# Performance work log

Hardware: AMD Instinct MI355X
Metric: run time of the kernel (lower is better)

Reference implementation:

```python
import jax, jax.numpy as jnp
import numpy as np

ALPHA = 1.0
BETA = 6.0
GAMMA = 1.0
N_DATA = 50000
IS_MSS = True
LOG2PI = float(np.log(2.0 * np.pi))


def _log_density_gaussian(x, mu, logvar):
    # elementwise Gaussian log-density
    return -0.5 * (LOG2PI + logvar) - 0.5 * (x - mu) ** 2 * jnp.exp(-logvar)


def _log_importance_weight_matrix(batch_size, n_data):
    # Faithful to the reference torch implementation (incl. the column-1 and
    # [M-1,0] stratified-weight overwrites done via flat strided assignment).
    N = float(n_data)
    M = float(batch_size - 1)
    strat = (N - M) / (N * M)
    W = jnp.full((batch_size, batch_size), 1.0 / M, dtype=jnp.float32)
    idx = jnp.arange(batch_size)
    W = W.at[idx, idx].set(1.0 / N)
    W = W.at[:, 1].set(strat)
    W = W.at[batch_size - 2, 0].set(strat)
    return jnp.log(W)


def setup_inputs() -> dict:
    key = jax.random.key(0)
    k1, k2, k3, k4, k5 = jax.random.split(key, 5)
    B, D = 1024, 64
    return {
        "recon_x": jax.random.normal(k1, (B, 3, 64, 64), dtype=jnp.float32),
        "x": jax.random.normal(k2, (B, 3, 64, 64), dtype=jnp.float32),
        "mu": jax.random.normal(k3, (B, D), dtype=jnp.float32),
        "logvar": jax.random.normal(k4, (B, D), dtype=jnp.float32),
        "noise": jax.random.normal(k5, (B, D), dtype=jnp.float32),
    }


def reference(recon_x, x, mu, logvar, noise):
    B, D = mu.shape
    # reconstruction: MSE with sum reduction
    reconstruction_loss = jnp.sum((recon_x - x) ** 2)

    # reparameterized latent sample (noise supplied deterministically)
    z = mu + noise * jnp.exp(0.5 * logvar)

    # log q(z|x) and log p(z), each summed over latent dims -> [B]
    log_q_zCx = _log_density_gaussian(z, mu, logvar).sum(axis=1)
    log_pz = _log_density_gaussian(z, jnp.zeros_like(z), jnp.zeros_like(z)).sum(axis=1)

    # pairwise matrix log q(z_i | x_j): [B, B, D]
    mat_log_qz = _log_density_gaussian(z[:, None, :], mu[None, :, :], logvar[None, :, :])
    if IS_MSS:
        log_iw = _log_importance_weight_matrix(B, N_DATA)
        mat_log_qz = mat_log_qz + log_iw[:, :, None]

    log_qz = jax.scipy.special.logsumexp(mat_log_qz.sum(axis=2), axis=1)  # [B]
    log_prod_qzi = jax.scipy.special.logsumexp(mat_log_qz, axis=1).sum(axis=1)  # [B]

    mi_loss = jnp.mean(log_q_zCx - log_qz)
    tc_loss = jnp.mean(log_qz - log_prod_qzi)
    dw_kl_loss = jnp.mean(log_prod_qzi - log_pz)

    return reconstruction_loss + (ALPHA * mi_loss + BETA * tc_loss + GAMMA * dw_kl_loss)
```

## Files before the change

kernel.cpp:

```cpp
#include <hip/hip_runtime.h>
#include <math.h>

typedef __attribute__((ext_vector_type(8))) short short8;
typedef __attribute__((ext_vector_type(4))) float f32x4;

#define BB 1024
#define DD 64
#define NPIX (1024*3*64*64)

#define LN2PI_F  1.8378770664093453f
#define LOG2E_F  1.4426950408889634f

#define INV_M  (1.0f/1023.0f)
#define INV_N  (1.0f/50000.0f)
#define STRATF ((float)((50000.0-1023.0)/(50000.0*1023.0)))
#define NEGBIG (-3.0e38f)

#define L2_INVM  (-9.9985904f)
#define L2_INVN  (-15.6096405f)
#define L2_STRAT (-10.0284195f)

#define WS_RP    0
#define WS_LQC   2048
#define WS_LPZ   3072
#define WS_LQZ   4096
#define WS_LPR   5120
#define WS_Z     6144
#define WS_Z2    71680
#define WS_A     137216
#define WS_B     202752
#define WS_C     268288
#define WS_KC    333824
#define WS_QZP   334848
#define WS_SEDP  400384
#define WS_ABF   924672
#define WS_BBF   990208

#define NB_RECON 1536
#define NB_PREP  256
#define RECON_REPS 8

#define NB_MM    256
#define NB_SED   1024

__device__ __forceinline__ float fexp2(float x){ return __builtin_amdgcn_exp2f(x); }
__device__ __forceinline__ float flog2(float x){ return __builtin_amdgcn_logf(x); }
__device__ __forceinline__ unsigned short tobf(float f){
    unsigned int u = __float_as_uint(f);
    u = (u + 0x7FFFu + ((u >> 16) & 1u)) >> 16;
    return (unsigned short)u;
}
__device__ __forceinline__ unsigned long long ld_agent(const unsigned long long* p) {
    return __hip_atomic_load(p, __ATOMIC_RELAXED, __HIP_MEMORY_SCOPE_AGENT);
}

__global__ __launch_bounds__(256) void k_reconprep(const float* __restrict__ rx,
                                                   const float* __restrict__ x,
                                                   const float* __restrict__ mu,
                                                   const float* __restrict__ logvar,
                                                   const float* __restrict__ noise,
                                                   float* __restrict__ ws) {
    int bid = blockIdx.x, t = threadIdx.x;
    if (bid < NB_RECON) {
        int gid = bid * 256 + t;
        const int stride = NB_RECON * 256;
        const unsigned long long* rp = (const unsigned long long*)rx;
        const unsigned long long* xp = (const unsigned long long*)x;
        float acc = 0.f;
        #pragma unroll
        for (int rep = 0; rep < RECON_REPS; rep++) {
            long long i2 = 2LL * (gid + rep * stride);
            unsigned long long a0 = ld_agent(rp + i2);
            unsigned long long a1 = ld_agent(rp + i2 + 1);
            unsigned long long b0 = ld_agent(xp + i2);
            unsigned long long b1 = ld_agent(xp + i2 + 1);
            float d0 = __uint_as_float((unsigned)a0)         - __uint_as_float((unsigned)b0);
            float d1 = __uint_as_float((unsigned)(a0 >> 32)) - __uint_as_float((unsigned)(b0 >> 32));
            float d2 = __uint_as_float((unsigned)a1)         - __uint_as_float((unsigned)b1);
            float d3 = __uint_as_float((unsigned)(a1 >> 32)) - __uint_as_float((unsigned)(b1 >> 32));
            acc = fmaf(d0, d0, acc); acc = fmaf(d1, d1, acc);
            acc = fmaf(d2, d2, acc); acc = fmaf(d3, d3, acc);
        }
        __shared__ float red[256];
        red[t] = acc; __syncthreads();
        for (int o = 128; o > 0; o >>= 1) {
            if (t < o) red[t] += red[t + o];
            __syncthreads();
        }
        if (t == 0) ws[WS_RP + bid] = red[0];
    } else {
        int pb = bid - NB_RECON;
        int d = t & 63, w = t >> 6;
        int i = pb * 4 + w;
        int idx = i * 64 + d;
        float m = mu[idx], lvv = logvar[idx], n = noise[idx];
        float sh   = fexp2(0.5f * LOG2E_F * lvv);
        float z    = fmaf(n, sh, m);
        float eneg = fexp2(-LOG2E_F * lvv);
        float a = -0.5f * LOG2E_F * eneg;
        float b = -2.0f * a * m;
        float c = fmaf(a, m * m, -0.5f * LOG2E_F * (LN2PI_F + lvv));
        float z2 = z * z;
        ws[WS_Z  + idx] = z;  ws[WS_Z2 + idx] = z2;
        ws[WS_A  + idx] = a;  ws[WS_B  + idx] = b;  ws[WS_C + idx] = c;
        unsigned short* abf = (unsigned short*)(ws + WS_ABF);
        unsigned short* bbf = (unsigned short*)(ws + WS_BBF);
        abf[i * 128 + d]      = tobf(z2);
        abf[i * 128 + 64 + d] = tobf(z);
        bbf[i * 128 + d]      = tobf(a);
        bbf[i * 128 + 64 + d] = tobf(b);
        float lqc = -0.5f * (LN2PI_F + lvv + n * n);
        float lpz = -0.5f * (LN2PI_F + z2);
        float kc  = c;
        for (int off = 32; off > 0; off >>= 1) {
            lqc += __shfl_xor(lqc, off, 64);
            lpz += __shfl_xor(lpz, off, 64);
            kc  += __shfl_xor(kc,  off, 64);
        }
        if (d == 0) { ws[WS_LQC + i] = lqc; ws[WS_LPZ + i] = lpz; ws[WS_KC + i] = kc; }
    }
}

__global__ __launch_bounds__(256) void k_pair(float* __restrict__ ws) {
    __shared__ float smem_f[2048];
    int bid = blockIdx.x, t = threadIdx.x;
    int lane = t & 63, w = t >> 6;
    if (bid < NB_MM) {
        const unsigned short* abf = (const unsigned short*)(ws + WS_ABF);
        const unsigned short* bbf = (const unsigned short*)(ws + WS_BBF);
        int i0 = (bid & 15) * 64, j0 = (bid >> 4) * 64;
        int lo = lane & 15, g = lane >> 4;
        int wi = (w >> 1) * 32, wj = (w & 1) * 32;
        f32x4 acc[2][2] = {};
        #pragma unroll
        for (int kk = 0; kk < 4; kk++) {
            short8 af[2], bfr[2];
            #pragma unroll
            for (int fy = 0; fy < 2; fy++)
                af[fy] = *(const short8*)&abf[(i0 + wi + fy * 16 + lo) * 128 + (kk * 4 + g) * 8];
            #pragma unroll
            for (int fx = 0; fx < 2; fx++)
                bfr[fx] = *(const short8*)&bbf[(j0 + wj + fx * 16 + lo) * 128 + (kk * 4 + g) * 8];
            #pragma unroll
            for (int fy = 0; fy < 2; fy++)
                #pragma unroll
                for (int fx = 0; fx < 2; fx++)
                    acc[fy][fx] = __builtin_amdgcn_mfma_f32_16x16x32_bf16(af[fy], bfr[fx], acc[fy][fx], 0, 0, 0);
        }
        int jA = j0 + wj + lo;
        float kcv0 = ws[WS_KC + jA], kcv1 = ws[WS_KC + jA + 16];
        int pc = (j0 >> 5) + (w & 1);
        #pragma unroll
        for (int fy = 0; fy < 2; fy++) {
            #pragma unroll
            for (int r = 0; r < 4; r++) {
                int i = i0 + wi + fy * 16 + g * 4 + r;
                float vv0, vv1;
                {
                    int j = jA;
                    float lw = (j == 1) ? L2_STRAT : (i == j) ? L2_INVN
                             : (i == 1022 && j == 0) ? L2_STRAT : L2_INVM;
                    vv0 = acc[fy][0][r] + kcv0 + 64.0f * lw;
                }
                {
                    int j = jA + 16;
                    float lw = (j == 1) ? L2_STRAT : (i == j) ? L2_INVN
                             : (i == 1022 && j == 0) ? L2_STRAT : L2_INVM;
                    vv1 = acc[fy][1][r] + kcv1 + 64.0f * lw;
                }
                float m = fmaxf(vv0, vv1);
                float s = fexp2(vv0 - m) + fexp2(vv1 - m);
                for (int off = 1; off < 16; off <<= 1) {
                    float om = __shfl_xor(m, off, 64);
                    float os = __shfl_xor(s, off, 64);
                    float M = fmaxf(m, om);
                    s = s * fexp2(m - M) + os * fexp2(om - M);
                    m = M;
                }
                if (lo == 0) {
                    ws[WS_QZP + ((pc << 10) + i) * 2]     = m;
                    ws[WS_QZP + ((pc << 10) + i) * 2 + 1] = s;
                }
            }
        }
    } else {
        int sid = bid - NB_MM;
        int ic = sid & 127, jc = sid >> 7;
        int i0 = ic * 8, d = lane;
        int jbase = jc * 128 + w * 32;
        const float* Ap = ws + WS_A;
        const float* Bp = ws + WS_B;
        const float* Cp = ws + WS_C;
        float z2r[8], zr[8], se[8];
        #pragma unroll
        for (int k = 0; k < 8; k++) {
            z2r[k] = ws[WS_Z2 + (i0 + k) * 64 + d];
            zr[k]  = ws[WS_Z  + (i0 + k) * 64 + d];
            se[k] = 0.f;
        }
        float aP[8], bP[8], cP[8], aQ[8], bQ[8], cQ[8];
        #pragma unroll
        for (int u = 0; u < 8; u++) {
            int gg = (jbase + u) * 64 + d;
            aP[u] = Ap[gg]; bP[u] = Bp[gg]; cP[u] = Cp[gg];
        }
        #pragma unroll
        for (int batch = 0; batch < 4; batch++) {
            if (batch < 3) {
                #pragma unroll
                for (int u = 0; u < 8; u++) {
                    int gg = (jbase + (batch + 1) * 8 + u) * 64 + d;
                    aQ[u] = Ap[gg]; bQ[u] = Bp[gg]; cQ[u] = Cp[gg];
                }
            }
            #pragma unroll
            for (int u = 0; u < 8; u++) {
                #pragma unroll
                for (int k = 0; k < 8; k++) {
                    float uu = fmaf(aP[u], z2r[k], fmaf(bP[u], zr[k], cP[u]));
                    se[k] += fexp2(uu);
                }
            }
            if (batch < 3) {
                #pragma unroll
                for (int u = 0; u < 8; u++) { aP[u] = aQ[u]; bP[u] = bQ[u]; cP[u] = cQ[u]; }
            }
        }
        float* sacc = smem_f;
        #pragma unroll
        for (int k = 0; k < 8; k++) sacc[w * 512 + k * 64 + d] = se[k];
        __syncthreads();
        int k0 = w * 2;
        for (int k = k0; k < k0 + 2; k++) {
            float tot = sacc[k * 64 + d] + sacc[512 + k * 64 + d]
                      + sacc[1024 + k * 64 + d] + sacc[1536 + k * 64 + d];
            ws[WS_SEDP + ((jc << 10) + i0 + k) * 64 + d] = tot;
        }
    }
}

__global__ __launch_bounds__(256) void k_post(float* __restrict__ ws) {
    int t = threadIdx.x, lane = t & 63, w = t >> 6;
    int i = blockIdx.x * 4 + w;
    float m = NEGBIG, s = 0.f;
    if (lane < 32) {
        m = ws[WS_QZP + ((lane << 10) + i) * 2];
        s = ws[WS_QZP + ((lane << 10) + i) * 2 + 1];
    }
    for (int off = 1; off < 64; off <<= 1) {
        float om = __shfl_xor(m, off, 64);
        float os = __shfl_xor(s, off, 64);
        float M = fmaxf(m, om);
        s = s * fexp2(m - M) + os * fexp2(om - M);
        m = M;
    }
    if (lane == 0) ws[WS_LQZ + i] = (m + flog2(s)) * (1.0f / LOG2E_F);
    int d = lane;
    float se = 0.f;
    for (int c = 0; c < 8; c++) se += ws[WS_SEDP + ((c << 10) + i) * 64 + d];
    float z2 = ws[WS_Z2 + i * 64 + d], z = ws[WS_Z + i * 64 + d];
    auto E = [&](int j) -> float {
        int gidx = j * 64 + d;
        return fexp2(fmaf(ws[WS_A + gidx], z2, fmaf(ws[WS_B + gidx], z, ws[WS_C + gidx])));
    };
    float sid = INV_M * se;
    if (i != 1)    sid += (INV_N  - INV_M) * E(i);
    sid += (STRATF - INV_M) * E(1);
    if (i == 1022) sid += (STRATF - INV_M) * E(0);
    float lg = flog2(sid);
    for (int off = 1; off < 64; off <<= 1) lg += __shfl_xor(lg, off, 64);
    if (d == 0) ws[WS_LPR + i] = lg * (1.0f / LOG2E_F);
}

__global__ __launch_bounds__(256) void k_final(const float* __restrict__ ws,
                                               float* __restrict__ out) {
    int t = threadIdx.x;
    float a0 = 0, a1 = 0, a2 = 0, a3 = 0, a4 = 0;
    for (int idx = t; idx < NB_RECON; idx += 256) a0 += ws[WS_RP + idx];
    for (int idx = t; idx < BB; idx += 256) {
        a1 += ws[WS_LQC + idx];
        a2 += ws[WS_LPZ + idx];
        a3 += ws[WS_LQZ + idx];
        a4 += ws[WS_LPR + idx];
    }
    __shared__ float red[256];
    float vals[5] = {a0, a1, a2, a3, a4};
    float res[5];
    for (int q = 0; q < 5; q++) {
        red[t] = vals[q]; __syncthreads();
        for (int o = 128; o > 0; o >>= 1) {
            if (t < o) red[t] += red[t + o];
            __syncthreads();
        }
        res[q] = red[0]; __syncthreads();
    }
    if (t == 0) {
        float recon = res[0], slqc = res[1], slpz = res[2], slqz = res[3], slpr = res[4];
        out[0] = recon + (slqc + 5.f * (slqz - slpr) - slpz) * (1.0f / (float)BB);
    }
}

extern "C" void kernel_launch(void* const* d_in, const int* in_sizes, int n_in,
                              void* d_out, int out_size, void* d_ws, size_t ws_size,
                              hipStream_t stream) {
    (void)in_sizes; (void)n_in; (void)out_size; (void)ws_size;
    const float* rx = (const float*)d_in[0];
    const float* x  = (const float*)d_in[1];
    const float* mu = (const float*)d_in[2];
    const float* lv = (const float*)d_in[3];
    const float* nz = (const float*)d_in[4];
    float* ws  = (float*)d_ws;
    float* out = (float*)d_out;

    k_reconprep<<<NB_RECON + NB_PREP, 256, 0, stream>>>(rx, x, mu, lv, nz, ws);
    k_pair     <<<NB_MM + NB_SED, 256, 0, stream>>>(ws);
    k_post     <<<256, 256, 0, stream>>>(ws);
    k_final    <<<1, 256, 0, stream>>>(ws, out);
}
```

Baseline: 47.36 us.

## Split reconstruction reduction into three chunks co-scheduled with pair stages

Splits the memory-bound MSE reduction into three chunks, each fused into a launch alongside prep, the pair/MFMA stage, and the post stage. The aim is to overlap the bandwidth-heavy recon streaming with the compute-bound pairwise work, so neither the recon pass nor the small prep/post kernels run alone on the GPU. The risk is that recon blocks compete with the MFMA and SED blocks for CUs within the same launch, and that the larger shared-memory allocation in k_d2 lowers occupancy for its recon blocks.

After: 45.30 us. -4.4%, faster.

```diff
diff --git a/kernel.cpp b/kernel.cpp
--- a/kernel.cpp
+++ b/kernel.cpp
@@ -36,12 +36,15 @@
 #define WS_ABF   924672
 #define WS_BBF   990208
 
-#define NB_RECON 1536
+#define RECON_CHUNK_BLOCKS 512
+#define RECON_CHUNK_F4     1048576
+#define RECON_CHUNK_THREADS (RECON_CHUNK_BLOCKS*256)
+#define RECON_REPS 8
+
 #define NB_PREP  256
-#define RECON_REPS 8
-
 #define NB_MM    256
 #define NB_SED   1024
+#define NB_POST  256
 
 __device__ __forceinline__ float fexp2(float x){ return __builtin_amdgcn_exp2f(x); }
 __device__ __forceinline__ float flog2(float x){ return __builtin_amdgcn_logf(x); }
@@ -54,194 +57,189 @@
     return __hip_atomic_load(p, __ATOMIC_RELAXED, __HIP_MEMORY_SCOPE_AGENT);
 }
 
-__global__ __launch_bounds__(256) void k_reconprep(const float* __restrict__ rx,
-                                                   const float* __restrict__ x,
-                                                   const float* __restrict__ mu,
-                                                   const float* __restrict__ logvar,
-                                                   const float* __restrict__ noise,
-                                                   float* __restrict__ ws) {
-    int bid = blockIdx.x, t = threadIdx.x;
-    if (bid < NB_RECON) {
-        int gid = bid * 256 + t;
-        const int stride = NB_RECON * 256;
-        const unsigned long long* rp = (const unsigned long long*)rx;
-        const unsigned long long* xp = (const unsigned long long*)x;
-        float acc = 0.f;
-        #pragma unroll
-        for (int rep = 0; rep < RECON_REPS; rep++) {
-            long long i2 = 2LL * (gid + rep * stride);
-            unsigned long long a0 = ld_agent(rp + i2);
-            unsigned long long a1 = ld_agent(rp + i2 + 1);
-            unsigned long long b0 = ld_agent(xp + i2);
-            unsigned long long b1 = ld_agent(xp + i2 + 1);
-            float d0 = __uint_as_float((unsigned)a0)         - __uint_as_float((unsigned)b0);
-            float d1 = __uint_as_float((unsigned)(a0 >> 32)) - __uint_as_float((unsigned)(b0 >> 32));
-            float d2 = __uint_as_float((unsigned)a1)         - __uint_as_float((unsigned)b1);
-            float d3 = __uint_as_float((unsigned)(a1 >> 32)) - __uint_as_float((unsigned)(b1 >> 32));
-            acc = fmaf(d0, d0, acc); acc = fmaf(d1, d1, acc);
-            acc = fmaf(d2, d2, acc); acc = fmaf(d3, d3, acc);
-        }
-        __shared__ float red[256];
-        red[t] = acc; __syncthreads();
-        for (int o = 128; o > 0; o >>= 1) {
-            if (t < o) red[t] += red[t + o];
-            __syncthreads();
-        }
-        if (t == 0) ws[WS_RP + bid] = red[0];
-    } else {
-        int pb = bid - NB_RECON;
-        int d = t & 63, w = t >> 6;
-        int i = pb * 4 + w;
-        int idx = i * 64 + d;
-        float m = mu[idx], lvv = logvar[idx], n = noise[idx];
-        float sh   = fexp2(0.5f * LOG2E_F * lvv);
-        float z    = fmaf(n, sh, m);
-        float eneg = fexp2(-LOG2E_F * lvv);
-        float a = -0.5f * LOG2E_F * eneg;
-        float b = -2.0f * a * m;
-        float c = fmaf(a, m * m, -0.5f * LOG2E_F * (LN2PI_F + lvv));
-        float z2 = z * z;
-        ws[WS_Z  + idx] = z;  ws[WS_Z2 + idx] = z2;
-        ws[WS_A  + idx] = a;  ws[WS_B  + idx] = b;  ws[WS_C + idx] = c;
-        unsigned short* abf = (unsigned short*)(ws + WS_ABF);
-        unsigned short* bbf = (unsigned short*)(ws + WS_BBF);
-        abf[i * 128 + d]      = tobf(z2);
-        abf[i * 128 + 64 + d] = tobf(z);
-        bbf[i * 128 + d]      = tobf(a);
-        bbf[i * 128 + 64 + d] = tobf(b);
-        float lqc = -0.5f * (LN2PI_F + lvv + n * n);
-        float lpz = -0.5f * (LN2PI_F + z2);
-        float kc  = c;
-        for (int off = 32; off > 0; off >>= 1) {
-            lqc += __shfl_xor(lqc, off, 64);
-            lpz += __shfl_xor(lpz, off, 64);
-            kc  += __shfl_xor(kc,  off, 64);
-        }
-        if (d == 0) { ws[WS_LQC + i] = lqc; ws[WS_LPZ + i] = lpz; ws[WS_KC + i] = kc; }
-    }
-}
-
-__global__ __launch_bounds__(256) void k_pair(float* __restrict__ ws) {
-    __shared__ float smem_f[2048];
-    int bid = blockIdx.x, t = threadIdx.x;
+__device__ __forceinline__ void do_recon(int chunk, int lb, int t,
+                                         const unsigned long long* rp,
+                                         const unsigned long long* xp,
+                                         float* __restrict__ ws,
+                                         float* __restrict__ red) {
+    long long base4 = (long long)chunk * RECON_CHUNK_F4 + lb * 256 + t;
+    float acc = 0.f;
+    #pragma unroll
+    for (int rep = 0; rep < RECON_REPS; rep++) {
+        long long i2 = 2LL * (base4 + rep * RECON_CHUNK_THREADS);
+        unsigned long long a0 = ld_agent(rp + i2);
+        unsigned long long a1 = ld_agent(rp + i2 + 1);
+        unsigned long long b0 = ld_agent(xp + i2);
+        unsigned long long b1 = ld_agent(xp + i2 + 1);
+        float d0 = __uint_as_float((unsigned)a0)         - __uint_as_float((unsigned)b0);
+        float d1 = __uint_as_float((unsigned)(a0 >> 32)) - __uint_as_float((unsigned)(b0 >> 32));
+        float d2 = __uint_as_float((unsigned)a1)         - __uint_as_float((unsigned)b1);
+        float d3 = __uint_as_float((unsigned)(a1 >> 32)) - __uint_as_float((unsigned)(b1 >> 32));
+        acc = fmaf(d0, d0, acc); acc = fmaf(d1, d1, acc);
+        acc = fmaf(d2, d2, acc); acc = fmaf(d3, d3, acc);
+    }
+    red[t] = acc; __syncthreads();
+    for (int o = 128; o > 0; o >>= 1) {
+        if (t < o) red[t] += red[t + o];
+        __syncthreads();
+    }
+    if (t == 0) ws[WS_RP + chunk * RECON_CHUNK_BLOCKS + lb] = red[0];
+}
+
+__device__ __forceinline__ void do_prep(int pb, int t,
+                                        const float* __restrict__ mu,
+                                        const float* __restrict__ logvar,
+                                        const float* __restrict__ noise,
+                                        float* __restrict__ ws) {
+    int d = t & 63, w = t >> 6;
+    int i = pb * 4 + w;
+    int idx = i * 64 + d;
+    float m = mu[idx], lvv = logvar[idx], n = noise[idx];
+    float sh   = fexp2(0.5f * LOG2E_F * lvv);
+    float z    = fmaf(n, sh, m);
+    float eneg = fexp2(-LOG2E_F * lvv);
+    float a = -0.5f * LOG2E_F * eneg;
+    float b = -2.0f * a * m;
+    float c = fmaf(a, m * m, -0.5f * LOG2E_F * (LN2PI_F + lvv));
+    float z2 = z * z;
+    ws[WS_Z  + idx] = z;  ws[WS_Z2 + idx] = z2;
+    ws[WS_A  + idx] = a;  ws[WS_B  + idx] = b;  ws[WS_C + idx] = c;
+    unsigned short* abf = (unsigned short*)(ws + WS_ABF);
+    unsigned short* bbf = (unsigned short*)(ws + WS_BBF);
+    abf[i * 128 + d]      = tobf(z2);
+    abf[i * 128 + 64 + d] = tobf(z);
+    bbf[i * 128 + d]      = tobf(a);
+    bbf[i * 128 + 64 + d] = tobf(b);
+    float lqc = -0.5f * (LN2PI_F + lvv + n * n);
+    float lpz = -0.5f * (LN2PI_F + z2);
+    float kc  = c;
+    for (int off = 32; off > 0; off >>= 1) {
+        lqc += __shfl_xor(lqc, off, 64);
+        lpz += __shfl_xor(lpz, off, 64);
+        kc  += __shfl_xor(kc,  off, 64);
+    }
+    if (d == 0) { ws[WS_LQC + i] = lqc; ws[WS_LPZ + i] = lpz; ws[WS_KC + i] = kc; }
+}
+
+__device__ __forceinline__ void do_mm(int mmid, int t, float* __restrict__ ws) {
     int lane = t & 63, w = t >> 6;
-    if (bid < NB_MM) {
-        const unsigned short* abf = (const unsigned short*)(ws + WS_ABF);
-        const unsigned short* bbf = (const unsigned short*)(ws + WS_BBF);
-        int i0 = (bid & 15) * 64, j0 = (bid >> 4) * 64;
-        int lo = lane & 15, g = lane >> 4;
-        int wi = (w >> 1) * 32, wj = (w & 1) * 32;
-        f32x4 acc[2][2] = {};
-        #pragma unroll
-        for (int kk = 0; kk < 4; kk++) {
-            short8 af[2], bfr[2];
-            #pragma unroll
-            for (int fy = 0; fy < 2; fy++)
-                af[fy] = *(const short8*)&abf[(i0 + wi + fy * 16 + lo) * 128 + (kk * 4 + g) * 8];
+    const unsigned short* abf = (const unsigned short*)(ws + WS_ABF);
+    const unsigned short* bbf = (const unsigned short*)(ws + WS_BBF);
+    int i0 = (mmid & 15) * 64, j0 = (mmid >> 4) * 64;
+    int lo = lane & 15, g = lane >> 4;
+    int wi = (w >> 1) * 32, wj = (w & 1) * 32;
+    f32x4 acc[2][2] = {};
+    #pragma unroll
+    for (int kk = 0; kk < 4; kk++) {
+        short8 af[2], bfr[2];
+        #pragma unroll
+        for (int fy = 0; fy < 2; fy++)
+            af[fy] = *(const short8*)&abf[(i0 + wi + fy * 16 + lo) * 128 + (kk * 4 + g) * 8];
+        #pragma unroll
+        for (int fx = 0; fx < 2; fx++)
+            bfr[fx] = *(const short8*)&bbf[(j0 + wj + fx * 16 + lo) * 128 + (kk * 4 + g) * 8];
+        #pragma unroll
+        for (int fy = 0; fy < 2; fy++)
             #pragma unroll
             for (int fx = 0; fx < 2; fx++)
-                bfr[fx] = *(const short8*)&bbf[(j0 + wj + fx * 16 + lo) * 128 + (kk * 4 + g) * 8];
-            #pragma unroll
-            for (int fy = 0; fy < 2; fy++)
-                #pragma unroll
-                for (int fx = 0; fx < 2; fx++)
-                    acc[fy][fx] = __builtin_amdgcn_mfma_f32_16x16x32_bf16(af[fy], bfr[fx], acc[fy][fx], 0, 0, 0);
-        }
-        int jA = j0 + wj + lo;
-        float kcv0 = ws[WS_KC + jA], kcv1 = ws[WS_KC + jA + 16];
-        int pc = (j0 >> 5) + (w & 1);
-        #pragma unroll
-        for (int fy = 0; fy < 2; fy++) {
-            #pragma unroll
-            for (int r = 0; r < 4; r++) {
-                int i = i0 + wi + fy * 16 + g * 4 + r;
-                float vv0, vv1;
-                {
-                    int j = jA;
-                    float lw = (j == 1) ? L2_STRAT : (i == j) ? L2_INVN
-                             : (i == 1022 && j == 0) ? L2_STRAT : L2_INVM;
-                    vv0 = acc[fy][0][r] + kcv0 + 64.0f * lw;
-                }
-                {
-                    int j = jA + 16;
-                    float lw = (j == 1) ? L2_STRAT : (i == j) ? L2_INVN
-                             : (i == 1022 && j == 0) ? L2_STRAT : L2_INVM;
-                    vv1 = acc[fy][1][r] + kcv1 + 64.0f * lw;
-                }
-                float m = fmaxf(vv0, vv1);
-                float s = fexp2(vv0 - m) + fexp2(vv1 - m);
-                for (int off = 1; off < 16; off <<= 1) {
-                    float om = __shfl_xor(m, off, 64);
-                    float os = __shfl_xor(s, off, 64);
-                    float M = fmaxf(m, om);
-                    s = s * fexp2(m - M) + os * fexp2(om - M);
-                    m = M;
-                }
-                if (lo == 0) {
-                    ws[WS_QZP + ((pc << 10) + i) * 2]     = m;
-                    ws[WS_QZP + ((pc << 10) + i) * 2 + 1] = s;
-                }
-            }
-        }
-    } else {
-        int sid = bid - NB_MM;
-        int ic = sid & 127, jc = sid >> 7;
-        int i0 = ic * 8, d = lane;
-        int jbase = jc * 128 + w * 32;
-        const float* Ap = ws + WS_A;
-        const float* Bp = ws + WS_B;
-        const float* Cp = ws + WS_C;
-        float z2r[8], zr[8], se[8];
-        #pragma unroll
-        for (int k = 0; k < 8; k++) {
-            z2r[k] = ws[WS_Z2 + (i0 + k) * 64 + d];
-            zr[k]  = ws[WS_Z  + (i0 + k) * 64 + d];
-            se[k] = 0.f;
-        }
-        float aP[8], bP[8], cP[8], aQ[8], bQ[8], cQ[8];
-        #pragma unroll
-        for (int u = 0; u < 8; u++) {
-            int gg = (jbase + u) * 64 + d;
-            aP[u] = Ap[gg]; bP[u] = Bp[gg]; cP[u] = Cp[gg];
-        }
-        #pragma unroll
-        for (int batch = 0; batch < 4; batch++) {
-            if (batch < 3) {
-                #pragma unroll
-                for (int u = 0; u < 8; u++) {
-                    int gg = (jbase + (batch + 1) * 8 + u) * 64 + d;
-                    aQ[u] = Ap[gg]; bQ[u] = Bp[gg]; cQ[u] = Cp[gg];
-                }
-            }
+                acc[fy][fx] = __builtin_amdgcn_mfma_f32_16x16x32_bf16(af[fy], bfr[fx], acc[fy][fx], 0, 0, 0);
+    }
+    int jA = j0 + wj + lo;
+    float kcv0 = ws[WS_KC + jA], kcv1 = ws[WS_KC + jA + 16];
+    int pc = (j0 >> 5) + (w & 1);
+    #pragma unroll
+    for (int fy = 0; fy < 2; fy++) {
+        #pragma unroll
+        for (int r = 0; r < 4; r++) {
+            int i = i0 + wi + fy * 16 + g * 4 + r;
+            float vv0, vv1;
+            {
+                int j = jA;
+                float lw = (j == 1) ? L2_STRAT : (i == j) ? L2_INVN
+                         : (i == 1022 && j == 0) ? L2_STRAT : L2_INVM;
+                vv0 = acc[fy][0][r] + kcv0 + 64.0f * lw;
+            }
+            {
+                int j = jA + 16;
+                float lw = (j == 1) ? L2_STRAT : (i == j) ? L2_INVN
+                         : (i == 1022 && j == 0) ? L2_STRAT : L2_INVM;
+                vv1 = acc[fy][1][r] + kcv1 + 64.0f * lw;
+            }
+            float m = fmaxf(vv0, vv1);
+            float s = fexp2(vv0 - m) + fexp2(vv1 - m);
+            for (int off = 1; off < 16; off <<= 1) {
+                float om = __shfl_xor(m, off, 64);
+                float os = __shfl_xor(s, off, 64);
+                float M = fmaxf(m, om);
+                s = s * fexp2(m - M) + os * fexp2(om - M);
+                m = M;
+            }
+            if (lo == 0) {
+                ws[WS_QZP + ((pc << 10) + i) * 2]     = m;
+                ws[WS_QZP + ((pc << 10) + i) * 2 + 1] = s;
+            }
+        }
+    }
+}
+
+__device__ __forceinline__ void do_sed(int sid, int t, float* __restrict__ ws,
+                                       float* __restrict__ sacc) {
+    int lane = t & 63, w = t >> 6;
+    int ic = sid & 127, jc = sid >> 7;
+    int i0 = ic * 8, d = lane;
+    int jbase = jc * 128 + w * 32;
+    const float* Ap = ws + WS_A;
+    const float* Bp = ws + WS_B;
+    const float* Cp = ws + WS_C;
+    float z2r[8], zr[8], se[8];
+    #pragma unroll
+    for (int k = 0; k < 8; k++) {
+        z2r[k] = ws[WS_Z2 + (i0 + k) * 64 + d];
+        zr[k]  = ws[WS_Z  + (i0 + k) * 64 + d];
+        se[k] = 0.f;
+    }
+    float aP[8], bP[8], cP[8], aQ[8], bQ[8], cQ[8];
+    #pragma unroll
+    for (int u = 0; u < 8; u++) {
+        int gg = (jbase + u) * 64 + d;
+        aP[u] = Ap[gg]; bP[u] = Bp[gg]; cP[u] = Cp[gg];
+    }
+    #pragma unroll
+    for (int batch = 0; batch < 4; batch++) {
+        if (batch < 3) {
             #pragma unroll
             for (int u = 0; u < 8; u++) {
-                #pragma unroll
-                for (int k = 0; k < 8; k++) {
-                    float uu = fmaf(aP[u], z2r[k], fmaf(bP[u], zr[k], cP[u]));
-                    se[k] += fexp2(uu);
-                }
-            }
-            if (batch < 3) {
-                #pragma unroll
-                for (int u = 0; u < 8; u++) { aP[u] = aQ[u]; bP[u] = bQ[u]; cP[u] = cQ[u]; }
-            }
-        }
-        float* sacc = smem_f;
-        #pragma unroll
-        for (int k = 0; k < 8; k++) sacc[w * 512 + k * 64 + d] = se[k];
-        __syncthreads();
-        int k0 = w * 2;
-        for (int k = k0; k < k0 + 2; k++) {
-            float tot = sacc[k * 64 + d] + sacc[512 + k * 64 + d]
-                      + sacc[1024 + k * 64 + d] + sacc[1536 + k * 64 + d];
-            ws[WS_SEDP + ((jc << 10) + i0 + k) * 64 + d] = tot;
-        }
-    }
-}
-
-__global__ __launch_bounds__(256) void k_post(float* __restrict__ ws) {
-    int t = threadIdx.x, lane = t & 63, w = t >> 6;
-    int i = blockIdx.x * 4 + w;
+                int gg = (jbase + (batch + 1) * 8 + u) * 64 + d;
+                aQ[u] = Ap[gg]; bQ[u] = Bp[gg]; cQ[u] = Cp[gg];
+            }
+        }
+        #pragma unroll
+        for (int u = 0; u < 8; u++) {
+            #pragma unroll
+            for (int k = 0; k < 8; k++) {
+                float uu = fmaf(aP[u], z2r[k], fmaf(bP[u], zr[k], cP[u]));
+                se[k] += fexp2(uu);
+            }
+        }
+        if (batch < 3) {
+            #pragma unroll
+            for (int u = 0; u < 8; u++) { aP[u] = aQ[u]; bP[u] = bQ[u]; cP[u] = cQ[u]; }
+        }
+    }
+    #pragma unroll
+    for (int k = 0; k < 8; k++) sacc[w * 512 + k * 64 + d] = se[k];
+    __syncthreads();
+    int k0 = w * 2;
+    for (int k = k0; k < k0 + 2; k++) {
+        float tot = sacc[k * 64 + d] + sacc[512 + k * 64 + d]
+                  + sacc[1024 + k * 64 + d] + sacc[1536 + k * 64 + d];
+        ws[WS_SEDP + ((jc << 10) + i0 + k) * 64 + d] = tot;
+    }
+}
+
+__device__ __forceinline__ void do_post(int pb, int t, float* __restrict__ ws) {
+    int lane = t & 63, w = t >> 6;
+    int i = pb * 4 + w;
     float m = NEGBIG, s = 0.f;
     if (lane < 32) {
         m = ws[WS_QZP + ((lane << 10) + i) * 2];
@@ -272,11 +270,49 @@
     if (d == 0) ws[WS_LPR + i] = lg * (1.0f / LOG2E_F);
 }
 
+__global__ __launch_bounds__(256) void k_d1(const float* __restrict__ rx,
+                                            const float* __restrict__ x,
+                                            const float* __restrict__ mu,
+                                            const float* __restrict__ logvar,
+                                            const float* __restrict__ noise,
+                                            float* __restrict__ ws) {
+    __shared__ float smem[256];
+    int bid = blockIdx.x, t = threadIdx.x;
+    if (bid < RECON_CHUNK_BLOCKS)
+        do_recon(0, bid, t, (const unsigned long long*)rx, (const unsigned long long*)x, ws, smem);
+    else
+        do_prep(bid - RECON_CHUNK_BLOCKS, t, mu, logvar, noise, ws);
+}
+
+__global__ __launch_bounds__(256) void k_d2(const float* __restrict__ rx,
+                                            const float* __restrict__ x,
+                                            float* __restrict__ ws) {
+    __shared__ float smem[2048];
+    int bid = blockIdx.x, t = threadIdx.x;
+    if (bid < RECON_CHUNK_BLOCKS)
+        do_recon(1, bid, t, (const unsigned long long*)rx, (const unsigned long long*)x, ws, smem);
+    else if (bid < RECON_CHUNK_BLOCKS + NB_MM)
+        do_mm(bid - RECON_CHUNK_BLOCKS, t, ws);
+    else
+        do_sed(bid - RECON_CHUNK_BLOCKS - NB_MM, t, ws, smem);
+}
+
+__global__ __launch_bounds__(256) void k_d3(const float* __restrict__ rx,
+                                            const float* __restrict__ x,
+                                            float* __restrict__ ws) {
+    __shared__ float smem[256];
+    int bid = blockIdx.x, t = threadIdx.x;
+    if (bid < RECON_CHUNK_BLOCKS)
+        do_recon(2, bid, t, (const unsigned long long*)rx, (const unsigned long long*)x, ws, smem);
+    else
+        do_post(bid - RECON_CHUNK_BLOCKS, t, ws);
+}
+
 __global__ __launch_bounds__(256) void k_final(const float* __restrict__ ws,
                                                float* __restrict__ out) {
     int t = threadIdx.x;
     float a0 = 0, a1 = 0, a2 = 0, a3 = 0, a4 = 0;
-    for (int idx = t; idx < NB_RECON; idx += 256) a0 += ws[WS_RP + idx];
+    for (int idx = t; idx < 1536; idx += 256) a0 += ws[WS_RP + idx];
     for (int idx = t; idx < BB; idx += 256) {
         a1 += ws[WS_LQC + idx];
         a2 += ws[WS_LPZ + idx];
@@ -312,8 +348,8 @@
     float* ws  = (float*)d_ws;
     float* out = (float*)d_out;
 
-    k_reconprep<<<NB_RECON + NB_PREP, 256, 0, stream>>>(rx, x, mu, lv, nz, ws);
-    k_pair     <<<NB_MM + NB_SED, 256, 0, stream>>>(ws);
-    k_post     <<<256, 256, 0, stream>>>(ws);
-    k_final    <<<1, 256, 0, stream>>>(ws, out);
-}
+    k_d1   <<<RECON_CHUNK_BLOCKS + NB_PREP,          256, 0, stream>>>(rx, x, mu, lv, nz, ws);
+    k_d2   <<<RECON_CHUNK_BLOCKS + NB_MM + NB_SED,   256, 0, stream>>>(rx, x, ws);
+    k_d3   <<<RECON_CHUNK_BLOCKS + NB_POST,          256, 0, stream>>>(rx, x, ws);
+    k_final<<<1, 256, 0, stream>>>(ws, out);
+}
```
